# Optimization experiments

Measured on AMD Instinct MI355X. Metric: run time of the kernel, lower is better.

The kernel has to match this reference:

```python
import jax, jax.numpy as jnp
import numpy as np

D_MODEL = 1024
D_INDEX = 32
NUM_HEADS = 4
SEQ_LEN = 4096
BATCH = 2


def setup_inputs() -> dict:
    key = jax.random.key(0)
    ks = jax.random.split(key, 7)
    s = 1.0 / np.sqrt(D_MODEL)
    x = jax.random.normal(ks[0], (SEQ_LEN, BATCH, D_MODEL), dtype=jnp.float32)
    Wq = jax.random.uniform(ks[1], (D_MODEL, NUM_HEADS * D_INDEX), jnp.float32, -s, s)
    bq = jax.random.uniform(ks[2], (NUM_HEADS * D_INDEX,), jnp.float32, -s, s)
    Wk = jax.random.uniform(ks[3], (D_MODEL, D_INDEX), jnp.float32, -s, s)
    bk = jax.random.uniform(ks[4], (D_INDEX,), jnp.float32, -s, s)
    Ww = jax.random.uniform(ks[5], (D_MODEL, NUM_HEADS), jnp.float32, -s, s)
    bw = jax.random.uniform(ks[6], (NUM_HEADS,), jnp.float32, -s, s)
    return {"x": x, "Wq": Wq, "bq": bq, "Wk": Wk, "bk": bk, "Ww": Ww, "bw": bw}


def reference(x, Wq, bq, Wk, bk, Ww, bw):
    # x: [T, B, D] -> batch-first [B, T, D]
    xb = jnp.transpose(x, (1, 0, 2))
    B, T, _ = xb.shape
    q = (xb @ Wq + bq).reshape(B, T, NUM_HEADS, D_INDEX)  # [B,T,H,d]
    k = xb @ Wk + bk                                       # [B,T,d] (keys over s)
    w = xb @ Ww + bw                                       # [B,T,H]
    dot = jnp.einsum('bthd,bsd->btsh', q, k)               # [B,T,S,H]
    activated = jax.nn.relu(dot)
    # sum over heads weighted by w[b,t,h]
    index_scores = jnp.einsum('btsh,bth->bts', activated, w)
    return index_scores
```

## Files before the change

kernel.cpp:

```cpp
#include <hip/hip_runtime.h>

#define T_SEQ 4096
#define NBATCH 2
#define DM 1024
#define DI 32
#define NH 4
#define NCOLS 164
#define NCOLS_PAD 192
#define KC 64
#define BSTRIDE 72

typedef __attribute__((ext_vector_type(8))) short bf16x8;
typedef __attribute__((ext_vector_type(4))) float f32x4;

__device__ __forceinline__ unsigned short f2bf(float f) {
    unsigned int u = __builtin_bit_cast(unsigned int, f);
    u += 0x7FFFu + ((u >> 16) & 1u);
    return (unsigned short)(u >> 16);
}

__global__ __launch_bounds__(256) void prep_kernel(
    const float* __restrict__ Wq, const float* __restrict__ bq,
    const float* __restrict__ Wk, const float* __restrict__ bk,
    const float* __restrict__ Ww, const float* __restrict__ bw,
    unsigned short* __restrict__ WT2, float* __restrict__ bias) {
    int c = blockIdx.x;
    const float* src = nullptr; int stride = 0; float bv = 0.f;
    if (c < 128)      { src = Wq + c;       stride = NH * DI; bv = bq[c]; }
    else if (c < 160) { src = Wk + (c-128); stride = DI;      bv = bk[c-128]; }
    else if (c < 164) { src = Ww + (c-160); stride = NH;      bv = bw[c-160]; }
    for (int k = threadIdx.x; k < DM; k += blockDim.x) {
        float v = src ? src[(size_t)k * stride] : 0.f;
        WT2[((size_t)(k >> 6) * NCOLS_PAD + c) * KC + (k & 63)] = f2bf(v);
    }
    if (threadIdx.x == 0) bias[c] = bv;
}

__global__ __launch_bounds__(512) void proj_kernel(
    const float* __restrict__ x, const unsigned short* __restrict__ WT2,
    const float* __restrict__ bias,
    unsigned short* __restrict__ qws, unsigned short* __restrict__ kws,
    float* __restrict__ wws) {
    __shared__ unsigned short Bb[2][NCOLS_PAD * BSTRIDE];
    __shared__ unsigned short Ab[2][2048];
    int t = threadIdx.x;
    int wave = t >> 6, lane = t & 63;
    int lr = lane & 15, kg = lane >> 4;
    int r0 = blockIdx.x * 32;

    int ahalf = t & 1, alane = (t >> 1) & 63, akk = (t >> 7) & 1, arh = t >> 8;
    int arow = r0 + arh * 16 + (alane & 15);
    int tA = arow & (T_SEQ - 1), bA = arow >> 12;
    const float* xrowA = x + ((size_t)tA * NBATCH + bA) * DM;
    int aoff = akk * 32 + (alane >> 4) * 8 + ahalf * 4;
    int adst = arh * 1024 + akk * 512 + alane * 8 + ahalf * 4;

    bf16x8 bregA[3], bregB[3];
    f32x4  aregA, aregB;

    auto LOADA = [&](int c) {
        const unsigned short* wp = WT2 + (size_t)c * (NCOLS_PAD * KC);
        #pragma unroll
        for (int it = 0; it < 3; ++it)
            bregA[it] = *(const bf16x8*)(wp + (it * 512 + t) * 8);
        aregA = *(const f32x4*)(xrowA + c * KC + aoff);
    };
    auto LOADB = [&](int c) {
        const unsigned short* wp = WT2 + (size_t)c * (NCOLS_PAD * KC);
        #pragma unroll
        for (int it = 0; it < 3; ++it)
            bregB[it] = *(const bf16x8*)(wp + (it * 512 + t) * 8);
        aregB = *(const f32x4*)(xrowA + c * KC + aoff);
    };
    auto WRITEA = [&](int buf) {
        #pragma unroll
        for (int it = 0; it < 3; ++it) {
            int tau = it * 512 + t;
            *(bf16x8*)(&Bb[buf][(tau >> 3) * BSTRIDE + (tau & 7) * 8]) = bregA[it];
        }
        unsigned short* d = &Ab[buf][adst];
        d[0] = f2bf(aregA[0]); d[1] = f2bf(aregA[1]);
        d[2] = f2bf(aregA[2]); d[3] = f2bf(aregA[3]);
    };
    auto WRITEB = [&](int buf) {
        #pragma unroll
        for (int it = 0; it < 3; ++it) {
            int tau = it * 512 + t;
            *(bf16x8*)(&Bb[buf][(tau >> 3) * BSTRIDE + (tau & 7) * 8]) = bregB[it];
        }
        unsigned short* d = &Ab[buf][adst];
        d[0] = f2bf(aregB[0]); d[1] = f2bf(aregB[1]);
        d[2] = f2bf(aregB[2]); d[3] = f2bf(aregB[3]);
    };

    int ct0 = (wave >> 1) * 3;
    int rh  = wave & 1;
    f32x4 acc[3] = {};

    auto COMPUTE = [&](int buf) {
        #pragma unroll
        for (int kk = 0; kk < 2; ++kk) {
            bf16x8 af = *(const bf16x8*)(&Ab[buf][rh * 1024 + kk * 512 + lane * 8]);
            #pragma unroll
            for (int i = 0; i < 3; ++i) {
                int col = (ct0 + i) * 16 + lr;
                bf16x8 bfg = *(const bf16x8*)(&Bb[buf][col * BSTRIDE + kk * 32 + kg * 8]);
                acc[i] = __builtin_amdgcn_mfma_f32_16x16x32_bf16(af, bfg, acc[i], 0, 0, 0);
            }
        }
    };

    LOADA(0);
    WRITEA(0);
    LOADB(1);
    __syncthreads();

    for (int c = 0; c < 16; c += 2) {
        if (c + 2 < 16) LOADA(c + 2);
        COMPUTE(0);
        __syncthreads();
        WRITEB(1);
        __syncthreads();
        if (c + 3 < 16) LOADB(c + 3);
        COMPUTE(1);
        __syncthreads();
        if (c + 2 < 16) WRITEA(0);
        __syncthreads();
    }

    #pragma unroll
    for (int i = 0; i < 3; ++i) {
        int cout = (ct0 + i) * 16 + lr;
        float bv = bias[cout];
        #pragma unroll
        for (int r = 0; r < 4; ++r) {
            int rr = r0 + rh * 16 + kg * 4 + r;
            int tt = rr & (T_SEQ - 1), bb = rr >> 12;
            float v = acc[i][r] + bv;
            size_t rowoff = (size_t)bb * T_SEQ + tt;
            if (cout < 128)       qws[rowoff * 128 + cout] = f2bf(v);
            else if (cout < 160)  kws[rowoff * 32 + (cout - 128)] = f2bf(v);
            else if (cout < 164)  wws[rowoff * 4 + (cout - 160)] = v;
        }
    }
}

__global__ __launch_bounds__(256) void indexer_kernel(
    const unsigned short* __restrict__ qws, const unsigned short* __restrict__ kws,
    const float* __restrict__ wws, float* __restrict__ out) {
    int wave = threadIdx.x >> 6;
    int lane = threadIdx.x & 63;
    int gw = blockIdx.x * 4 + wave;
    int strip = gw & 15;
    int t16 = (gw >> 4) & 255;
    int b = gw >> 12;
    int t0 = t16 * 16;
    int lr = lane & 15, kg = lane >> 4;

    const unsigned short* qrow = qws + ((size_t)b * T_SEQ + t0 + lr) * 128;
    bf16x8 qf[4];
    #pragma unroll
    for (int h = 0; h < 4; ++h)
        qf[h] = *(const bf16x8*)(qrow + h * 32 + kg * 8);

    f32x4 w4 = *(const f32x4*)(wws + ((size_t)b * T_SEQ + t0 + lr) * 4);

    float* outrow = out + (size_t)b * T_SEQ * T_SEQ + (size_t)(t0 + lr) * T_SEQ;
    const unsigned short* kbase = kws + (size_t)b * T_SEQ * 32;
    int sbase = strip * 256;

    for (int g = 0; g < 4; ++g) {
        int s0 = sbase + g * 64;
        bf16x8 kf0 = *(const bf16x8*)(kbase + (size_t)(s0      + lr) * 32 + kg * 8);
        bf16x8 kf1 = *(const bf16x8*)(kbase + (size_t)(s0 + 16 + lr) * 32 + kg * 8);
        bf16x8 kf2 = *(const bf16x8*)(kbase + (size_t)(s0 + 32 + lr) * 32 + kg * 8);
        bf16x8 kf3 = *(const bf16x8*)(kbase + (size_t)(s0 + 48 + lr) * 32 + kg * 8);
        f32x4 z = {0.f, 0.f, 0.f, 0.f};
        f32x4 v[4];
        #pragma unroll
        for (int j = 0; j < 4; ++j) {
            bf16x8 kf = (j == 0) ? kf0 : (j == 1) ? kf1 : (j == 2) ? kf2 : kf3;
            f32x4 a0 = __builtin_amdgcn_mfma_f32_16x16x32_bf16(kf, qf[0], z, 0, 0, 0);
            f32x4 a1 = __builtin_amdgcn_mfma_f32_16x16x32_bf16(kf, qf[1], z, 0, 0, 0);
            f32x4 a2 = __builtin_amdgcn_mfma_f32_16x16x32_bf16(kf, qf[2], z, 0, 0, 0);
            f32x4 a3 = __builtin_amdgcn_mfma_f32_16x16x32_bf16(kf, qf[3], z, 0, 0, 0);
            #pragma unroll
            for (int r = 0; r < 4; ++r) {
                v[j][r] = fmaxf(a0[r], 0.f) * w4[0] + fmaxf(a1[r], 0.f) * w4[1]
                        + fmaxf(a2[r], 0.f) * w4[2] + fmaxf(a3[r], 0.f) * w4[3];
            }
        }
        #pragma unroll
        for (int j = 0; j < 4; ++j)
            *(f32x4*)(outrow + s0 + j * 16 + kg * 4) = v[j];
    }
}

extern "C" void kernel_launch(void* const* d_in, const int* in_sizes, int n_in,
                              void* d_out, int out_size, void* d_ws, size_t ws_size,
                              hipStream_t stream) {
    const float* x  = (const float*)d_in[0];
    const float* Wq = (const float*)d_in[1];
    const float* bq = (const float*)d_in[2];
    const float* Wk = (const float*)d_in[3];
    const float* bk = (const float*)d_in[4];
    const float* Ww = (const float*)d_in[5];
    const float* bw = (const float*)d_in[6];
    float* out = (float*)d_out;

    char* ws = (char*)d_ws;
    unsigned short* WT2 = (unsigned short*)(ws);
    float* bias         = (float*)(ws + 393216);
    unsigned short* qws = (unsigned short*)(ws + 524288);
    unsigned short* kws = (unsigned short*)(ws + 2621440);
    float* wws          = (float*)(ws + 3145728);

    prep_kernel<<<dim3(NCOLS_PAD), dim3(256), 0, stream>>>(Wq, bq, Wk, bk, Ww, bw, WT2, bias);
    proj_kernel<<<dim3(256), dim3(512), 0, stream>>>(x, WT2, bias, qws, kws, wws);
    indexer_kernel<<<dim3(2048), dim3(256), 0, stream>>>(qws, kws, wws, out);
}
```

Before: 54.15 us.

## Stage key fragments in LDS and retile indexer blocks for key reuse

```diff
diff --git a/kernel.cpp b/kernel.cpp
--- a/kernel.cpp
+++ b/kernel.cpp
@@ -145,54 +145,68 @@
     }
 }
 
-__global__ __launch_bounds__(256) void indexer_kernel(
+__global__ __launch_bounds__(512) void indexer_kernel(
     const unsigned short* __restrict__ qws, const unsigned short* __restrict__ kws,
     const float* __restrict__ wws, float* __restrict__ out) {
-    int wave = threadIdx.x >> 6;
-    int lane = threadIdx.x & 63;
-    int gw = blockIdx.x * 4 + wave;
-    int strip = gw & 15;
-    int t16 = (gw >> 4) & 255;
-    int b = gw >> 12;
-    int t0 = t16 * 16;
+    __shared__ unsigned short kf_lds[16384];
+    int t = threadIdx.x;
+    int wave = t >> 6;
+    int lane = t & 63;
     int lr = lane & 15, kg = lane >> 4;
 
-    const unsigned short* qrow = qws + ((size_t)b * T_SEQ + t0 + lr) * 128;
+    int blk = blockIdx.x;
+    int b = blk >> 10;
+    int rem = blk & 1023;
+    int t32 = rem >> 3;
+    int sblk = rem & 7;
+    int t0 = t32 * 32;
+    int s0 = sblk * 512;
+
+    const unsigned short* kbase = kws + (size_t)b * T_SEQ * 32;
+
+    {
+        const unsigned short* krow = kbase + (size_t)(s0 + t) * 32;
+        int ldst = (t >> 4) * 512 + (t & 15) * 8;
+        #pragma unroll
+        for (int j = 0; j < 4; ++j) {
+            bf16x8 kv = *(const bf16x8*)(krow + j * 8);
+            *(bf16x8*)(&kf_lds[ldst + j * 128]) = kv;
+        }
+    }
+
+    int h = wave & 1;
+    int sq = wave >> 1;
+    int trow = t0 + h * 16;
+
+    const unsigned short* qrow = qws + ((size_t)b * T_SEQ + trow + lr) * 128;
     bf16x8 qf[4];
     #pragma unroll
-    for (int h = 0; h < 4; ++h)
-        qf[h] = *(const bf16x8*)(qrow + h * 32 + kg * 8);
-
-    f32x4 w4 = *(const f32x4*)(wws + ((size_t)b * T_SEQ + t0 + lr) * 4);
-
-    float* outrow = out + (size_t)b * T_SEQ * T_SEQ + (size_t)(t0 + lr) * T_SEQ;
-    const unsigned short* kbase = kws + (size_t)b * T_SEQ * 32;
-    int sbase = strip * 256;
-
-    for (int g = 0; g < 4; ++g) {
-        int s0 = sbase + g * 64;
-        bf16x8 kf0 = *(const bf16x8*)(kbase + (size_t)(s0      + lr) * 32 + kg * 8);
-        bf16x8 kf1 = *(const bf16x8*)(kbase + (size_t)(s0 + 16 + lr) * 32 + kg * 8);
-        bf16x8 kf2 = *(const bf16x8*)(kbase + (size_t)(s0 + 32 + lr) * 32 + kg * 8);
-        bf16x8 kf3 = *(const bf16x8*)(kbase + (size_t)(s0 + 48 + lr) * 32 + kg * 8);
+    for (int hh = 0; hh < 4; ++hh)
+        qf[hh] = *(const bf16x8*)(qrow + hh * 32 + kg * 8);
+
+    f32x4 w4 = *(const f32x4*)(wws + ((size_t)b * T_SEQ + trow + lr) * 4);
+
+    float* outrow = out + (size_t)b * T_SEQ * T_SEQ + (size_t)(trow + lr) * T_SEQ
+                  + s0 + sq * 128;
+
+    __syncthreads();
+
+    #pragma unroll 2
+    for (int st = 0; st < 8; ++st) {
+        int sl = sq * 8 + st;
+        bf16x8 kf = *(const bf16x8*)(&kf_lds[sl * 512 + lane * 8]);
         f32x4 z = {0.f, 0.f, 0.f, 0.f};
-        f32x4 v[4];
-        #pragma unroll
-        for (int j = 0; j < 4; ++j) {
-            bf16x8 kf = (j == 0) ? kf0 : (j == 1) ? kf1 : (j == 2) ? kf2 : kf3;
-            f32x4 a0 = __builtin_amdgcn_mfma_f32_16x16x32_bf16(kf, qf[0], z, 0, 0, 0);
-            f32x4 a1 = __builtin_amdgcn_mfma_f32_16x16x32_bf16(kf, qf[1], z, 0, 0, 0);
-            f32x4 a2 = __builtin_amdgcn_mfma_f32_16x16x32_bf16(kf, qf[2], z, 0, 0, 0);
-            f32x4 a3 = __builtin_amdgcn_mfma_f32_16x16x32_bf16(kf, qf[3], z, 0, 0, 0);
-            #pragma unroll
-            for (int r = 0; r < 4; ++r) {
-                v[j][r] = fmaxf(a0[r], 0.f) * w4[0] + fmaxf(a1[r], 0.f) * w4[1]
-                        + fmaxf(a2[r], 0.f) * w4[2] + fmaxf(a3[r], 0.f) * w4[3];
-            }
-        }
-        #pragma unroll
-        for (int j = 0; j < 4; ++j)
-            *(f32x4*)(outrow + s0 + j * 16 + kg * 4) = v[j];
+        f32x4 a0 = __builtin_amdgcn_mfma_f32_16x16x32_bf16(kf, qf[0], z, 0, 0, 0);
+        f32x4 a1 = __builtin_amdgcn_mfma_f32_16x16x32_bf16(kf, qf[1], z, 0, 0, 0);
+        f32x4 a2 = __builtin_amdgcn_mfma_f32_16x16x32_bf16(kf, qf[2], z, 0, 0, 0);
+        f32x4 a3 = __builtin_amdgcn_mfma_f32_16x16x32_bf16(kf, qf[3], z, 0, 0, 0);
+        f32x4 v;
+        #pragma unroll
+        for (int r = 0; r < 4; ++r) {
+            v[r] = fmaxf(a0[r], 0.f) * w4[0] + fmaxf(a1[r], 0.f) * w4[1]
+                 + fmaxf(a2[r], 0.f) * w4[2] + fmaxf(a3[r], 0.f) * w4[3];
+        }
+        *(f32x4*)(outrow + st * 16 + kg * 4) = v;
     }
 }
 
@@ -217,5 +231,5 @@
 
     prep_kernel<<<dim3(NCOLS_PAD), dim3(256), 0, stream>>>(Wq, bq, Wk, bk, Ww, bw, WT2, bias);
     proj_kernel<<<dim3(256), dim3(512), 0, stream>>>(x, WT2, bias, qws, kws, wws);
-    indexer_kernel<<<dim3(2048), dim3(256), 0, stream>>>(qws, kws, wws, out);
-}
+    indexer_kernel<<<dim3(2048), dim3(512), 0, stream>>>(qws, kws, wws, out);
+}
```

Measured after the change: 48.51 us. -10.4%, faster.
